# Performance work log

Hardware: AMD Instinct MI355X
Metric: run time of the kernel (lower is better)

The kernel has to match this reference:

```python
import jax, jax.numpy as jnp
import numpy as np

N, F, K = 2048, 256, 4
E = 65536

def setup_inputs() -> dict:
    key = jax.random.key(0)
    ks = jax.random.split(key, 8)
    batch_x = jax.random.normal(ks[0], (N, F), dtype=jnp.float32)
    # eigen-matrix of a normalized Laplacian is diagonal in practice, but the
    # original code treats it as a dense [N,N] operand; we mimic a diagonal
    # eigenvalue matrix (eigenvalues in [0,2]) -- math is identical either way.
    lam_diag = 2.0 * jax.random.uniform(ks[1], (N,), dtype=jnp.float32)
    batch_lam = jnp.diag(lam_diag)
    batch_U = jax.random.normal(ks[2], (N, N), dtype=jnp.float32) / jnp.sqrt(jnp.float32(N))
    # init.uniform_(a, 0, 2) / (b, 0, 2) / (c, -1, 1); keep a-b bounded away from 0
    a_list = 1.0 + jax.random.uniform(ks[3], (K,), dtype=jnp.float32)        # [1,2)
    b_list = 0.9 * jax.random.uniform(ks[4], (K,), dtype=jnp.float32)       # [0,0.9)
    c_list = 2.0 * jax.random.uniform(ks[5], (K,), dtype=jnp.float32) - 1.0  # [-1,1)
    residual_alpha = jnp.ones((1,), dtype=jnp.float32)
    edge_index = jax.random.randint(ks[6], (2, E), 0, N, dtype=jnp.int64)
    return {"batch_x": batch_x, "batch_lam": batch_lam, "batch_U": batch_U,
            "a_list": a_list, "b_list": b_list, "c_list": c_list,
            "residual_alpha": residual_alpha, "edge_index": edge_index}

def reference(batch_x, batch_lam, batch_U, a_list, b_list, c_list, residual_alpha, edge_index):
    n = batch_lam.shape[0]
    I = jnp.eye(n, dtype=batch_lam.dtype)
    out = residual_alpha * batch_x  # residual added at hop 0 in original
    for i in range(a_list.shape[0]):
        # filter_rep = (a_i*I - Lam) @ (Lam - b_i*I), then relu
        rep = (a_list[i] * I - batch_lam) @ (batch_lam - b_list[i] * I)
        rep = jax.nn.relu(rep)
        scale = c_list[i] / ((a_list[i] - b_list[i]) * (a_list[i] - b_list[i]) / 4.0)
        filt = scale * (batch_U @ (rep @ (batch_U.T @ batch_x)))
        out = out + filt
    return out
```

## Files before the change

kernel.cpp:

```cpp
#include <hip/hip_runtime.h>
#include <type_traits>

typedef unsigned short u16;
typedef __attribute__((ext_vector_type(8))) short short8;
typedef __attribute__((ext_vector_type(4))) float floatx4;

__device__ __forceinline__ u16 f2u(float f) {
  unsigned int x = __float_as_uint(f);
  x += 0x7fff + ((x >> 16) & 1);
  return (u16)(x >> 16);
}

__device__ __forceinline__ void async16(const void* g, void* l) {
  __builtin_amdgcn_global_load_lds(
      (const __attribute__((address_space(1))) unsigned int*)g,
      (__attribute__((address_space(3))) unsigned int*)l, 16, 0, 0);
}

__global__ __launch_bounds__(256) void prep_kernel(
    const float* __restrict__ U, const float* __restrict__ x,
    u16* __restrict__ Ut, u16* __restrict__ Ubf, u16* __restrict__ xT,
    int N, int F) {
  __shared__ __attribute__((aligned(16))) float tile[64][65];
  int bb = blockIdx.x;
  int t = threadIdx.x;

  const float* in;
  u16 *outT, *outC;
  int R, C, c0, r0;
  if (bb < 1024) {
    in = U; outT = Ut; outC = Ubf; R = N; C = N;
    c0 = (bb & 31) * 64; r0 = (bb >> 5) * 64;
  } else {
    int b2 = bb - 1024;
    in = x; outT = xT; outC = nullptr; R = N; C = F;
    c0 = (b2 & 3) * 64; r0 = (b2 >> 2) * 64;
  }

#pragma unroll
  for (int p = 0; p < 4; ++p) {
    int e = p * 256 + t;
    int row = e >> 4, col = (e & 15) * 4;
    float4 v = *(const float4*)(in + (size_t)(r0 + row) * C + c0 + col);
    tile[row][col] = v.x;
    tile[row][col + 1] = v.y;
    tile[row][col + 2] = v.z;
    tile[row][col + 3] = v.w;
    if (outC) {
      union { uint2 u; u16 s[4]; } pk;
      pk.s[0] = f2u(v.x); pk.s[1] = f2u(v.y);
      pk.s[2] = f2u(v.z); pk.s[3] = f2u(v.w);
      *(uint2*)(outC + (size_t)(r0 + row) * C + c0 + col) = pk.u;
    }
  }
  __syncthreads();
#pragma unroll
  for (int p = 0; p < 2; ++p) {
    int e = p * 256 + t;
    int orow = e >> 3, oc = (e & 7) * 8;
    union { uint4 v; u16 s[8]; } tmp;
#pragma unroll
    for (int i = 0; i < 8; ++i) tmp.s[i] = f2u(tile[oc + i][orow]);
    *(uint4*)(outT + (size_t)(c0 + orow) * R + r0 + oc) = tmp.v;
  }
}

template <bool SCALE_D, bool RESIDUAL, typename CT>
__global__ __launch_bounds__(256) void gemm32(
    const u16* __restrict__ A, const u16* __restrict__ B, CT* __restrict__ C,
    int M, int NN, int K, const float* __restrict__ lam,
    const float* __restrict__ pa, const float* __restrict__ pb,
    const float* __restrict__ pc, const float* __restrict__ resid,
    const float* __restrict__ alpha_p) {
  __shared__ __attribute__((aligned(16))) u16 lA[2 * 8192];
  __shared__ __attribute__((aligned(16))) u16 lB[2 * 8192];
  const int m0 = blockIdx.x * 32;
  const int n0 = blockIdx.y * 32;
  const int t = threadIdx.x;
  const int wave = t >> 6, lane = t & 63;
  const int wm = wave >> 1, wn = wave & 1;
  const int q = lane >> 4, l15 = lane & 15;

  const int within = t & 127, st0 = t >> 7;
  const u16* gA = A + (size_t)(m0 + (within >> 2)) * K + (within & 3) * 8;
  const u16* gB = B + (size_t)(n0 + (within >> 2)) * K + (within & 3) * 8;
  char* lAc = (char*)lA;
  char* lBc = (char*)lB;

  const int NM = K >> 8;

  auto issue = [&](int i, int buf) {
    int k0 = i * 256;
#pragma unroll
    for (int p = 0; p < 4; ++p) {
      int st = 2 * p + st0;
      async16(gA + k0 + st * 32, lAc + buf * 16384 + p * 4096 + t * 16);
      async16(gB + k0 + st * 32, lBc + buf * 16384 + p * 4096 + t * 16);
    }
  };

  floatx4 acc = (floatx4){0.f, 0.f, 0.f, 0.f};

  issue(0, 0);
  for (int i = 0; i < NM; ++i) {
    const int buf = i & 1;
    __syncthreads();
    if (i + 1 < NM) issue(i + 1, buf ^ 1);
    const u16* lAb = lA + buf * 8192;
    const u16* lBb = lB + buf * 8192;
#pragma unroll
    for (int st = 0; st < 8; ++st) {
      short8 af = *(const short8*)&lAb[st * 1024 + (wm * 16 + l15) * 32 + q * 8];
      short8 bf = *(const short8*)&lBb[st * 1024 + (wn * 16 + l15) * 32 + q * 8];
      acc = __builtin_amdgcn_mfma_f32_16x16x32_bf16(af, bf, acc, 0, 0, 0);
    }
  }

  const int col = n0 + wn * 16 + l15;
  float ds = 1.f;
  if (SCALE_D) {
    float lv = lam[(size_t)col * NN + col];
    float dacc = 0.f;
#pragma unroll
    for (int i = 0; i < 4; ++i) {
      float ai = pa[i], bi = pb[i], ci = pc[i];
      float rep = (ai - lv) * (lv - bi);
      rep = rep > 0.f ? rep : 0.f;
      dacc += ci * 4.f / ((ai - bi) * (ai - bi)) * rep;
    }
    ds = dacc;
  }
  float alpha = 0.f;
  if (RESIDUAL) alpha = alpha_p[0];
  const int rbase = m0 + wm * 16 + q * 4;
#pragma unroll
  for (int r = 0; r < 4; ++r) {
    float v = acc[r];
    if (SCALE_D) v *= ds;
    size_t idx = (size_t)(rbase + r) * NN + col;
    if (RESIDUAL) v += alpha * resid[idx];
    if constexpr (std::is_same<CT, u16>::value)
      C[idx] = f2u(v);
    else
      C[idx] = v;
  }
}

extern "C" void kernel_launch(void* const* d_in, const int* in_sizes, int n_in,
                              void* d_out, int out_size, void* d_ws,
                              size_t ws_size, hipStream_t stream) {
  const int N = 2048, F = 256;
  const float* x = (const float*)d_in[0];
  const float* lam = (const float*)d_in[1];
  const float* U = (const float*)d_in[2];
  const float* a = (const float*)d_in[3];
  const float* b = (const float*)d_in[4];
  const float* c = (const float*)d_in[5];
  const float* alpha = (const float*)d_in[6];

  char* ws = (char*)d_ws;
  u16* xT = (u16*)ws;
  u16* Ut = (u16*)(ws + (1 << 20));
  u16* Ubf = (u16*)(ws + (9 << 20));
  u16* zT = (u16*)(ws + (17 << 20));

  prep_kernel<<<1152, 256, 0, stream>>>(U, x, Ut, Ubf, xT, N, F);
  gemm32<true, false, u16><<<dim3(F / 32, N / 32), 256, 0, stream>>>(
      xT, Ut, zT, F, N, N, lam, a, b, c, nullptr, nullptr);
  gemm32<false, true, float><<<dim3(N / 32, F / 32), 256, 0, stream>>>(
      Ubf, zT, (float*)d_out, N, F, N, nullptr, nullptr, nullptr, nullptr,
      x, alpha);
}
```

Before: 109.8 us.

## Fuse prep and both GEMMs into one cooperative kernel with grid syncs

Replaces the three separate launches (conversion/transpose prep, first GEMM, second GEMM) with a single cooperative kernel of 512 blocks. The prep stage is grid-strided and the stages are separated by grid-wide barriers. The aim is to remove per-launch overhead and inter-kernel gaps. In exchange it adds grid-sync cost, caps the grid at 512 co-resident blocks, and enlarges shared memory to 64KB, which may limit occupancy.

```diff
diff --git a/kernel.cpp b/kernel.cpp
--- a/kernel.cpp
+++ b/kernel.cpp
@@ -1,5 +1,8 @@
 #include <hip/hip_runtime.h>
+#include <hip/hip_cooperative_groups.h>
 #include <type_traits>
+
+namespace cg = cooperative_groups;
 
 typedef unsigned short u16;
 typedef __attribute__((ext_vector_type(8))) short short8;
@@ -17,65 +20,13 @@
       (__attribute__((address_space(3))) unsigned int*)l, 16, 0, 0);
 }
 
-__global__ __launch_bounds__(256) void prep_kernel(
-    const float* __restrict__ U, const float* __restrict__ x,
-    u16* __restrict__ Ut, u16* __restrict__ Ubf, u16* __restrict__ xT,
-    int N, int F) {
-  __shared__ __attribute__((aligned(16))) float tile[64][65];
-  int bb = blockIdx.x;
-  int t = threadIdx.x;
-
-  const float* in;
-  u16 *outT, *outC;
-  int R, C, c0, r0;
-  if (bb < 1024) {
-    in = U; outT = Ut; outC = Ubf; R = N; C = N;
-    c0 = (bb & 31) * 64; r0 = (bb >> 5) * 64;
-  } else {
-    int b2 = bb - 1024;
-    in = x; outT = xT; outC = nullptr; R = N; C = F;
-    c0 = (b2 & 3) * 64; r0 = (b2 >> 2) * 64;
-  }
-
-#pragma unroll
-  for (int p = 0; p < 4; ++p) {
-    int e = p * 256 + t;
-    int row = e >> 4, col = (e & 15) * 4;
-    float4 v = *(const float4*)(in + (size_t)(r0 + row) * C + c0 + col);
-    tile[row][col] = v.x;
-    tile[row][col + 1] = v.y;
-    tile[row][col + 2] = v.z;
-    tile[row][col + 3] = v.w;
-    if (outC) {
-      union { uint2 u; u16 s[4]; } pk;
-      pk.s[0] = f2u(v.x); pk.s[1] = f2u(v.y);
-      pk.s[2] = f2u(v.z); pk.s[3] = f2u(v.w);
-      *(uint2*)(outC + (size_t)(r0 + row) * C + c0 + col) = pk.u;
-    }
-  }
-  __syncthreads();
-#pragma unroll
-  for (int p = 0; p < 2; ++p) {
-    int e = p * 256 + t;
-    int orow = e >> 3, oc = (e & 7) * 8;
-    union { uint4 v; u16 s[8]; } tmp;
-#pragma unroll
-    for (int i = 0; i < 8; ++i) tmp.s[i] = f2u(tile[oc + i][orow]);
-    *(uint4*)(outT + (size_t)(c0 + orow) * R + r0 + oc) = tmp.v;
-  }
-}
-
 template <bool SCALE_D, bool RESIDUAL, typename CT>
-__global__ __launch_bounds__(256) void gemm32(
-    const u16* __restrict__ A, const u16* __restrict__ B, CT* __restrict__ C,
-    int M, int NN, int K, const float* __restrict__ lam,
-    const float* __restrict__ pa, const float* __restrict__ pb,
-    const float* __restrict__ pc, const float* __restrict__ resid,
-    const float* __restrict__ alpha_p) {
-  __shared__ __attribute__((aligned(16))) u16 lA[2 * 8192];
-  __shared__ __attribute__((aligned(16))) u16 lB[2 * 8192];
-  const int m0 = blockIdx.x * 32;
-  const int n0 = blockIdx.y * 32;
+__device__ __forceinline__ void gemm32_body(
+    u16* lA, u16* lB, const u16* __restrict__ A, const u16* __restrict__ B,
+    CT* __restrict__ C, int M, int NN, int K, int m0, int n0,
+    const float* __restrict__ lam, const float* __restrict__ pa,
+    const float* __restrict__ pb, const float* __restrict__ pc,
+    const float* __restrict__ resid, float alpha) {
   const int t = threadIdx.x;
   const int wave = t >> 6, lane = t & 63;
   const int wm = wave >> 1, wn = wave & 1;
@@ -130,8 +81,6 @@
     }
     ds = dacc;
   }
-  float alpha = 0.f;
-  if (RESIDUAL) alpha = alpha_p[0];
   const int rbase = m0 + wm * 16 + q * 4;
 #pragma unroll
   for (int r = 0; r < 4; ++r) {
@@ -146,10 +95,90 @@
   }
 }
 
+__global__ __launch_bounds__(256) void mega_kernel(
+    const float* __restrict__ U, const float* __restrict__ x,
+    const float* __restrict__ lam, const float* __restrict__ a,
+    const float* __restrict__ b, const float* __restrict__ c,
+    const float* __restrict__ alpha_p, float* __restrict__ out,
+    u16* __restrict__ xT, u16* __restrict__ Ut, u16* __restrict__ Ubf,
+    u16* __restrict__ zT) {
+  __shared__ __attribute__((aligned(16))) char smem[65536];
+  const int t = threadIdx.x;
+  const int N = 2048, F = 256;
+
+  {
+    float(*tile)[65] = (float(*)[65])smem;
+    for (int bb = blockIdx.x; bb < 1152; bb += gridDim.x) {
+      const float* in;
+      u16 *outT, *outC;
+      int C_, c0, r0;
+      if (bb < 1024) {
+        in = U; outT = Ut; outC = Ubf; C_ = N;
+        c0 = (bb & 31) * 64; r0 = (bb >> 5) * 64;
+      } else {
+        int b2 = bb - 1024;
+        in = x; outT = xT; outC = nullptr; C_ = F;
+        c0 = (b2 & 3) * 64; r0 = (b2 >> 2) * 64;
+      }
+#pragma unroll
+      for (int p = 0; p < 4; ++p) {
+        int e = p * 256 + t;
+        int row = e >> 4, col = (e & 15) * 4;
+        float4 v = *(const float4*)(in + (size_t)(r0 + row) * C_ + c0 + col);
+        tile[row][col] = v.x;
+        tile[row][col + 1] = v.y;
+        tile[row][col + 2] = v.z;
+        tile[row][col + 3] = v.w;
+        if (outC) {
+          union { uint2 u; u16 s[4]; } pk;
+          pk.s[0] = f2u(v.x); pk.s[1] = f2u(v.y);
+          pk.s[2] = f2u(v.z); pk.s[3] = f2u(v.w);
+          *(uint2*)(outC + (size_t)(r0 + row) * C_ + c0 + col) = pk.u;
+        }
+      }
+      __syncthreads();
+#pragma unroll
+      for (int p = 0; p < 2; ++p) {
+        int e = p * 256 + t;
+        int orow = e >> 3, oc = (e & 7) * 8;
+        union { uint4 v; u16 s[8]; } tmp;
+#pragma unroll
+        for (int i = 0; i < 8; ++i) tmp.s[i] = f2u(tile[oc + i][orow]);
+        *(uint4*)(outT + (size_t)(c0 + orow) * N + r0 + oc) = tmp.v;
+      }
+      __syncthreads();
+    }
+  }
+
+  __threadfence();
+  cg::this_grid().sync();
+
+  {
+    u16* lA = (u16*)smem;
+    u16* lB = (u16*)(smem + 32768);
+    int m0 = (blockIdx.x & 7) * 32;
+    int n0 = (blockIdx.x >> 3) * 32;
+    gemm32_body<true, false, u16>(lA, lB, xT, Ut, zT, F, N, N, m0, n0,
+                                  lam, a, b, c, nullptr, 0.f);
+  }
+
+  __threadfence();
+  cg::this_grid().sync();
+
+  {
+    u16* lA = (u16*)smem;
+    u16* lB = (u16*)(smem + 32768);
+    int m0 = (blockIdx.x & 63) * 32;
+    int n0 = (blockIdx.x >> 6) * 32;
+    gemm32_body<false, true, float>(lA, lB, Ubf, zT, out, N, F, N, m0, n0,
+                                    nullptr, nullptr, nullptr, nullptr,
+                                    x, alpha_p[0]);
+  }
+}
+
 extern "C" void kernel_launch(void* const* d_in, const int* in_sizes, int n_in,
                               void* d_out, int out_size, void* d_ws,
                               size_t ws_size, hipStream_t stream) {
-  const int N = 2048, F = 256;
   const float* x = (const float*)d_in[0];
   const float* lam = (const float*)d_in[1];
   const float* U = (const float*)d_in[2];
@@ -163,11 +192,10 @@
   u16* Ut = (u16*)(ws + (1 << 20));
   u16* Ubf = (u16*)(ws + (9 << 20));
   u16* zT = (u16*)(ws + (17 << 20));
-
-  prep_kernel<<<1152, 256, 0, stream>>>(U, x, Ut, Ubf, xT, N, F);
-  gemm32<true, false, u16><<<dim3(F / 32, N / 32), 256, 0, stream>>>(
-      xT, Ut, zT, F, N, N, lam, a, b, c, nullptr, nullptr);
-  gemm32<false, true, float><<<dim3(N / 32, F / 32), 256, 0, stream>>>(
-      Ubf, zT, (float*)d_out, N, F, N, nullptr, nullptr, nullptr, nullptr,
-      x, alpha);
-}
+  float* outp = (float*)d_out;
+
+  void* args[] = {&U, &x, &lam, &a, &b, &c, &alpha, &outp,
+                  &xT, &Ut, &Ubf, &zT};
+  hipLaunchCooperativeKernel((const void*)mega_kernel, dim3(512), dim3(256),
+                             args, 0, stream);
+}
```

Result: slower. 340.9 us (+210.4%).
